# Performance work log

Hardware: AMD Instinct MI355X
Metric: run time of the kernel (lower is better)

## Reference

```python
import jax, jax.numpy as jnp
import numpy as np

DIM = 192
WH, WW = 8, 8
N = WH * WW
NUM_HEADS = 6
HEAD_DIM = DIM // NUM_HEADS
SCALE = HEAD_DIM ** (-0.5)
B_ = 4096


def _relative_position_index(Wh, Ww):
    coords = np.stack(np.meshgrid(np.arange(Wh), np.arange(Ww), indexing='ij'))  # [2, Wh, Ww]
    cf = coords.reshape(2, -1)                              # [2, N]
    rel = cf[:, :, None] - cf[:, None, :]                   # [2, N, N]
    rel = rel.transpose(1, 2, 0).astype(np.int64)           # [N, N, 2]
    rel[..., 0] += Wh - 1
    rel[..., 1] += Ww - 1
    rel[..., 0] *= 2 * Ww - 1
    return rel.sum(-1)                                      # [N, N]


REL_IDX = jnp.asarray(_relative_position_index(WH, WW))


def setup_inputs() -> dict:
    key = jax.random.key(0)
    ks = jax.random.split(key, 6)
    x = jax.random.normal(ks[0], (B_, N, DIM), dtype=jnp.float32)
    w_qkv = jax.random.normal(ks[1], (3 * DIM, DIM), dtype=jnp.float32) * (DIM ** -0.5)
    b_qkv = jnp.zeros((3 * DIM,), dtype=jnp.float32)
    w_proj = jax.random.normal(ks[2], (DIM, DIM), dtype=jnp.float32) * (DIM ** -0.5)
    b_proj = jnp.zeros((DIM,), dtype=jnp.float32)
    # torch init is zeros; use small noise so the bias path is exercised
    bias_table = jax.random.normal(ks[3], ((2 * WH - 1) * (2 * WW - 1), NUM_HEADS), dtype=jnp.float32) * 0.02
    return {"x": x, "w_qkv": w_qkv, "b_qkv": b_qkv, "w_proj": w_proj,
            "b_proj": b_proj, "bias_table": bias_table}


def reference(x, w_qkv, b_qkv, w_proj, b_proj, bias_table):
    B, n, C = x.shape
    qkv = jnp.einsum('bnc,dc->bnd', x, w_qkv) + b_qkv        # [B, N, 3C]
    qkv = qkv.reshape(B, n, 3, NUM_HEADS, HEAD_DIM)
    q = qkv[:, :, 0].transpose(0, 2, 1, 3) * SCALE            # [B, H, N, hd]
    k = qkv[:, :, 1].transpose(0, 2, 1, 3)
    v = qkv[:, :, 2].transpose(0, 2, 1, 3)
    attn = jnp.einsum('bhnd,bhmd->bhnm', q, k)                # [B, H, N, N]
    bias = bias_table[REL_IDX]                                # [N, N, H]
    attn = attn + bias.transpose(2, 0, 1)[None]               # broadcast over B
    attn = jax.nn.softmax(attn, axis=-1)
    out = jnp.einsum('bhnm,bhmd->bnhd', attn, v).reshape(B, n, C)
    return jnp.einsum('bnc,dc->bnd', out, w_proj) + b_proj
```

## Files before the change

kernel.cpp:

```cpp
#include <hip/hip_runtime.h>

#define TOK 64
#define CDIM 192
#define NH 6
#define HD 32
#define THREADS 384
#define QSCALE 0.17677669529663687f

#define WQ16_OFF 0
#define WP16_OFF 110592
#define BIAS_OFF 147456
#define WS_HALFS (147456 + 24576)
#define WS_BYTES (WS_HALFS * 2)

typedef _Float16 f16x8 __attribute__((ext_vector_type(8)));
typedef _Float16 f16x4 __attribute__((ext_vector_type(4)));
typedef float f32x4 __attribute__((ext_vector_type(4)));

__device__ __forceinline__ f16x8 ld8(const _Float16* p) {
  return *reinterpret_cast<const f16x8*>(p);
}

__device__ __forceinline__ f16x8 cvt8(const float* __restrict__ p) {
  float4 a = *reinterpret_cast<const float4*>(p);
  float4 c = *reinterpret_cast<const float4*>(p + 4);
  f16x8 r;
  r[0] = (_Float16)a.x; r[1] = (_Float16)a.y; r[2] = (_Float16)a.z; r[3] = (_Float16)a.w;
  r[4] = (_Float16)c.x; r[5] = (_Float16)c.y; r[6] = (_Float16)c.z; r[7] = (_Float16)c.w;
  return r;
}

__device__ __forceinline__ f16x4 pack4(float a, float b, float c, float d) {
  f16x4 r;
  r[0] = (_Float16)a; r[1] = (_Float16)b; r[2] = (_Float16)c; r[3] = (_Float16)d;
  return r;
}

__global__ void prep_ws(const float* __restrict__ wq, const float* __restrict__ wp,
                        const float* __restrict__ bt, _Float16* __restrict__ ws) {
  int i = blockIdx.x * 256 + threadIdx.x;
  if (i < 27648) {
    float4 v = reinterpret_cast<const float4*>(wq)[i];
    f16x4 h;
    h[0] = (_Float16)v.x; h[1] = (_Float16)v.y; h[2] = (_Float16)v.z; h[3] = (_Float16)v.w;
    *reinterpret_cast<f16x4*>(ws + WQ16_OFF + (size_t)i * 4) = h;
  } else if (i < 36864) {
    int j = i - 27648;
    float4 v = reinterpret_cast<const float4*>(wp)[j];
    f16x4 h;
    h[0] = (_Float16)v.x; h[1] = (_Float16)v.y; h[2] = (_Float16)v.z; h[3] = (_Float16)v.w;
    *reinterpret_cast<f16x4*>(ws + WP16_OFF + (size_t)j * 4) = h;
  } else if (i < 61440) {
    int j = i - 36864;
    int hit = j >> 10;
    int l = (j >> 4) & 63;
    int s = j & 15;
    int h = hit >> 2, it = hit & 3;
    int ii = it * 16 + (l & 15);
    int jj = (s >> 2) * 16 + (l >> 4) * 4 + (s & 3);
    int rel = ((ii >> 3) - (jj >> 3) + 7) * 15 + ((ii & 7) - (jj & 7) + 7);
    ws[BIAS_OFF + j] = (_Float16)bt[rel * NH + h];
  }
}

template <bool WS>
__global__ __launch_bounds__(THREADS, 5) void winattn(
    const float* __restrict__ x, const float* __restrict__ w_qkv,
    const float* __restrict__ b_qkv, const float* __restrict__ w_proj,
    const float* __restrict__ b_proj, const float* __restrict__ bias_table,
    const _Float16* __restrict__ ws, float* __restrict__ out) {
  __shared__ __align__(16) _Float16 R1[12288];

  const int tid = threadIdx.x;
  const int h   = tid >> 6;
  const int l   = tid & 63;
  const int l15 = l & 15;
  const int lg  = l >> 4;
  const int b   = blockIdx.x;
  const int sA0 = l15 ^ lg;
  const int sA1 = sA0 ^ 4;
  const f32x4 vzero = {0.f, 0.f, 0.f, 0.f};

  const float* xg = x + (size_t)b * (TOK * CDIM);
#pragma unroll
  for (int kk = 0; kk < 4; ++kk) {
    int q = tid + kk * THREADS;
    int n = q / 24;
    int p = q - n * 24;
    const float* src = xg + q * 8;
    float4 v0 = *reinterpret_cast<const float4*>(src);
    float4 v1 = *reinterpret_cast<const float4*>(src + 4);
    f16x8 h8;
    h8[0] = (_Float16)v0.x; h8[1] = (_Float16)v0.y;
    h8[2] = (_Float16)v0.z; h8[3] = (_Float16)v0.w;
    h8[4] = (_Float16)v1.x; h8[5] = (_Float16)v1.y;
    h8[6] = (_Float16)v1.z; h8[7] = (_Float16)v1.w;
    *reinterpret_cast<f16x8*>(&R1[(p * TOK + (n ^ (p & 7))) * 8]) = h8;
  }
  __syncthreads();

  f32x4 aq[2][4];
#pragma unroll
  for (int mt = 0; mt < 2; ++mt)
#pragma unroll
    for (int nt = 0; nt < 4; ++nt) aq[mt][nt] = vzero;
#pragma unroll
  for (int ks = 0; ks < 6; ++ks) {
    const int sx = (ks & 1) ? sA1 : sA0;
    f16x8 bx[4];
#pragma unroll
    for (int nt = 0; nt < 4; ++nt)
      bx[nt] = ld8(&R1[((ks * 4 + lg) * TOK + nt * 16 + sx) * 8]);
    f16x8 aw[2];
#pragma unroll
    for (int mt = 0; mt < 2; ++mt) {
      int row = h * HD + mt * 16 + l15;
      if constexpr (WS) aw[mt] = ld8(ws + WQ16_OFF + (size_t)row * CDIM + ks * 32 + lg * 8);
      else              aw[mt] = cvt8(w_qkv + (size_t)row * CDIM + ks * 32 + lg * 8);
    }
    __builtin_amdgcn_s_setprio(1);
#pragma unroll
    for (int mt = 0; mt < 2; ++mt)
#pragma unroll
      for (int nt = 0; nt < 4; ++nt)
        aq[mt][nt] = __builtin_amdgcn_mfma_f32_16x16x32_f16(aw[mt], bx[nt], aq[mt][nt], 0, 0, 0);
    __builtin_amdgcn_s_setprio(0);
  }
  f16x4 qp[2][4];
#pragma unroll
  for (int mt = 0; mt < 2; ++mt) {
    float4 bq = *reinterpret_cast<const float4*>(b_qkv + h * HD + mt * 16 + lg * 4);
#pragma unroll
    for (int nt = 0; nt < 4; ++nt)
      qp[mt][nt] = pack4((aq[mt][nt][0] + bq.x) * QSCALE, (aq[mt][nt][1] + bq.y) * QSCALE,
                         (aq[mt][nt][2] + bq.z) * QSCALE, (aq[mt][nt][3] + bq.w) * QSCALE);
  }

  f32x4 ak[2][4];
#pragma unroll
  for (int mt = 0; mt < 2; ++mt)
#pragma unroll
    for (int nt = 0; nt < 4; ++nt) ak[mt][nt] = vzero;
#pragma unroll
  for (int ks = 0; ks < 6; ++ks) {
    const int sx = (ks & 1) ? sA1 : sA0;
    f16x8 bx[4];
#pragma unroll
    for (int nt = 0; nt < 4; ++nt)
      bx[nt] = ld8(&R1[((ks * 4 + lg) * TOK + nt * 16 + sx) * 8]);
    f16x8 aw[2];
#pragma unroll
    for (int mt = 0; mt < 2; ++mt) {
      int row = CDIM + h * HD + mt * 16 + l15;
      if constexpr (WS) aw[mt] = ld8(ws + WQ16_OFF + (size_t)row * CDIM + ks * 32 + lg * 8);
      else              aw[mt] = cvt8(w_qkv + (size_t)row * CDIM + ks * 32 + lg * 8);
    }
    __builtin_amdgcn_s_setprio(1);
#pragma unroll
    for (int mt = 0; mt < 2; ++mt)
#pragma unroll
      for (int nt = 0; nt < 4; ++nt)
        ak[mt][nt] = __builtin_amdgcn_mfma_f32_16x16x32_f16(aw[mt], bx[nt], ak[mt][nt], 0, 0, 0);
    __builtin_amdgcn_s_setprio(0);
  }
  f16x4 kp[2][4];
#pragma unroll
  for (int mt = 0; mt < 2; ++mt) {
    float4 bk = *reinterpret_cast<const float4*>(b_qkv + CDIM + h * HD + mt * 16 + lg * 4);
#pragma unroll
    for (int nt = 0; nt < 4; ++nt)
      kp[mt][nt] = pack4(ak[mt][nt][0] + bk.x, ak[mt][nt][1] + bk.y,
                         ak[mt][nt][2] + bk.z, ak[mt][nt][3] + bk.w);
  }

  f16x4 vp[4][2];
#pragma unroll
  for (int ct = 0; ct < 2; ++ct) {
    f32x4 av[4];
#pragma unroll
    for (int mt = 0; mt < 4; ++mt) av[mt] = vzero;
    const int col = 2 * CDIM + h * HD + ct * 16 + l15;
#pragma unroll
    for (int ks = 0; ks < 6; ++ks) {
      const int sx = (ks & 1) ? sA1 : sA0;
      f16x8 a[4];
#pragma unroll
      for (int mt = 0; mt < 4; ++mt)
        a[mt] = ld8(&R1[((ks * 4 + lg) * TOK + mt * 16 + sx) * 8]);
      f16x8 bw;
      if constexpr (WS) bw = ld8(ws + WQ16_OFF + (size_t)col * CDIM + ks * 32 + lg * 8);
      else              bw = cvt8(w_qkv + (size_t)col * CDIM + ks * 32 + lg * 8);
      __builtin_amdgcn_s_setprio(1);
#pragma unroll
      for (int mt = 0; mt < 4; ++mt)
        av[mt] = __builtin_amdgcn_mfma_f32_16x16x32_f16(a[mt], bw, av[mt], 0, 0, 0);
      __builtin_amdgcn_s_setprio(0);
    }
    float bv = b_qkv[col];
#pragma unroll
    for (int s = 0; s < 4; ++s)
      vp[s][ct] = pack4(av[s][0] + bv, av[s][1] + bv, av[s][2] + bv, av[s][3] + bv);
  }
  __syncthreads();

#pragma unroll
  for (int it = 0; it < 4; ++it) {
    f32x4 st[4];
    __builtin_amdgcn_s_setprio(1);
#pragma unroll
    for (int jt = 0; jt < 4; ++jt) {
      st[jt] = __builtin_amdgcn_mfma_f32_16x16x16f16(kp[0][jt], qp[0][it], vzero, 0, 0, 0);
      st[jt] = __builtin_amdgcn_mfma_f32_16x16x16f16(kp[1][jt], qp[1][it], st[jt], 0, 0, 0);
    }
    __builtin_amdgcn_s_setprio(0);
    if constexpr (WS) {
      const _Float16* bw = ws + BIAS_OFF + ((h * 4 + it) * 64 + l) * 16;
      f16x8 b0 = ld8(bw), b1 = ld8(bw + 8);
#pragma unroll
      for (int jt = 0; jt < 4; ++jt)
#pragma unroll
        for (int r = 0; r < 4; ++r)
          st[jt][r] += (float)((jt < 2) ? b0[jt * 4 + r] : b1[(jt - 2) * 4 + r]);
    } else {
      int i = it * 16 + l15, yi = i >> 3, xi = i & 7;
#pragma unroll
      for (int jt = 0; jt < 4; ++jt)
#pragma unroll
        for (int r = 0; r < 4; ++r) {
          int j = jt * 16 + lg * 4 + r, yj = j >> 3, xj = j & 7;
          st[jt][r] += bias_table[(((yi - yj + 7) * 15 + (xi - xj + 7)) * NH + h)];
        }
    }
    float m = st[0][0];
#pragma unroll
    for (int jt = 0; jt < 4; ++jt)
#pragma unroll
      for (int r = 0; r < 4; ++r) m = fmaxf(m, st[jt][r]);
    m = fmaxf(m, __shfl_xor(m, 16, 64));
    m = fmaxf(m, __shfl_xor(m, 32, 64));
    float sum = 0.f;
#pragma unroll
    for (int jt = 0; jt < 4; ++jt)
#pragma unroll
      for (int r = 0; r < 4; ++r) { st[jt][r] = __expf(st[jt][r] - m); sum += st[jt][r]; }
    sum += __shfl_xor(sum, 16, 64);
    sum += __shfl_xor(sum, 32, 64);
    float inv = 1.f / sum;
    f32x4 o[2] = {vzero, vzero};
#pragma unroll
    for (int s = 0; s < 4; ++s) {
      f16x4 pp = pack4(st[s][0] * inv, st[s][1] * inv, st[s][2] * inv, st[s][3] * inv);
      __builtin_amdgcn_s_setprio(1);
      o[0] = __builtin_amdgcn_mfma_f32_16x16x16f16(pp, vp[s][0], o[0], 0, 0, 0);
      o[1] = __builtin_amdgcn_mfma_f32_16x16x16f16(pp, vp[s][1], o[1], 0, 0, 0);
      __builtin_amdgcn_s_setprio(0);
    }
#pragma unroll
    for (int ct = 0; ct < 2; ++ct) {
      int c = h * HD + ct * 16 + l15;
      int op = c >> 3, s7 = op & 7;
      int lgx = lg ^ (s7 >> 2);
      int base = (op * TOK + it * 16 + lgx * 4) * 8 + (c & 7);
#pragma unroll
      for (int r = 0; r < 4; ++r)
        R1[base + (r ^ (s7 & 3)) * 8] = (_Float16)o[ct][r];
    }
  }
  __syncthreads();

  {
    const int e0 = h * 16 + l15;
    const int e1 = e0 + 96;
    f32x4 pa0[4], pa1[4];
#pragma unroll
    for (int mt = 0; mt < 4; ++mt) { pa0[mt] = vzero; pa1[mt] = vzero; }
#pragma unroll
    for (int ks = 0; ks < 6; ++ks) {
      const int sx = (ks & 1) ? sA1 : sA0;
      f16x8 a[4];
#pragma unroll
      for (int mt = 0; mt < 4; ++mt)
        a[mt] = ld8(&R1[((ks * 4 + lg) * TOK + mt * 16 + sx) * 8]);
      f16x8 w0, w1;
      if constexpr (WS) {
        w0 = ld8(ws + WP16_OFF + (size_t)e0 * CDIM + ks * 32 + lg * 8);
        w1 = ld8(ws + WP16_OFF + (size_t)e1 * CDIM + ks * 32 + lg * 8);
      } else {
        w0 = cvt8(w_proj + (size_t)e0 * CDIM + ks * 32 + lg * 8);
        w1 = cvt8(w_proj + (size_t)e1 * CDIM + ks * 32 + lg * 8);
      }
      __builtin_amdgcn_s_setprio(1);
#pragma unroll
      for (int mt = 0; mt < 4; ++mt) {
        pa0[mt] = __builtin_amdgcn_mfma_f32_16x16x32_f16(a[mt], w0, pa0[mt], 0, 0, 0);
        pa1[mt] = __builtin_amdgcn_mfma_f32_16x16x32_f16(a[mt], w1, pa1[mt], 0, 0, 0);
      }
      __builtin_amdgcn_s_setprio(0);
    }
    float bp0 = b_proj[e0], bp1 = b_proj[e1];
#pragma unroll
    for (int mt = 0; mt < 4; ++mt) {
#pragma unroll
      for (int r = 0; r < 4; ++r) {
        int n = mt * 16 + lg * 4 + r;
        out[((size_t)b * TOK + n) * CDIM + e0] = pa0[mt][r] + bp0;
        out[((size_t)b * TOK + n) * CDIM + e1] = pa1[mt][r] + bp1;
      }
    }
  }
}

extern "C" void kernel_launch(void* const* d_in, const int* in_sizes, int n_in,
                              void* d_out, int out_size, void* d_ws, size_t ws_size,
                              hipStream_t stream) {
  const float* x          = (const float*)d_in[0];
  const float* w_qkv      = (const float*)d_in[1];
  const float* b_qkv      = (const float*)d_in[2];
  const float* w_proj     = (const float*)d_in[3];
  const float* b_proj     = (const float*)d_in[4];
  const float* bias_table = (const float*)d_in[5];
  float* out = (float*)d_out;
  int B = in_sizes[0] / (TOK * CDIM);

  if (ws_size >= (size_t)WS_BYTES) {
    _Float16* ws = (_Float16*)d_ws;
    hipLaunchKernelGGL(prep_ws, dim3(240), dim3(256), 0, stream,
                       w_qkv, w_proj, bias_table, ws);
    hipLaunchKernelGGL(winattn<true>, dim3(B), dim3(THREADS), 0, stream,
                       x, w_qkv, b_qkv, w_proj, b_proj, bias_table, ws, out);
  } else {
    hipLaunchKernelGGL(winattn<false>, dim3(B), dim3(THREADS), 0, stream,
                       x, w_qkv, b_qkv, w_proj, b_proj, bias_table,
                       (const _Float16*)nullptr, out);
  }
}
```

Before: 243.5 us.

## Fuse Q, K and V projection loops to share LDS x-fragment loads

Merges the three separate Q, K and V projection k-loops into one loop that loads the x tile fragments from LDS once per k-step and issues all 24 MFMAs against them. This cuts LDS reads of the activation tile to a third and gives the scheduler more independent MFMAs per iteration. In exchange all three accumulator sets are live at once, raising register pressure, so the launch-bounds occupancy hint is lowered from 5 to 3 blocks per CU.

```diff
diff --git a/kernel.cpp b/kernel.cpp
--- a/kernel.cpp
+++ b/kernel.cpp
@@ -64,7 +64,7 @@
 }
 
 template <bool WS>
-__global__ __launch_bounds__(THREADS, 5) void winattn(
+__global__ __launch_bounds__(THREADS, 3) void winattn(
     const float* __restrict__ x, const float* __restrict__ w_qkv,
     const float* __restrict__ b_qkv, const float* __restrict__ w_proj,
     const float* __restrict__ b_proj, const float* __restrict__ bias_table,
@@ -99,11 +99,16 @@
   }
   __syncthreads();
 
-  f32x4 aq[2][4];
+  f32x4 aq[2][4], ak[2][4], av[4][2];
 #pragma unroll
   for (int mt = 0; mt < 2; ++mt)
 #pragma unroll
-    for (int nt = 0; nt < 4; ++nt) aq[mt][nt] = vzero;
+    for (int nt = 0; nt < 4; ++nt) { aq[mt][nt] = vzero; ak[mt][nt] = vzero; }
+#pragma unroll
+  for (int mt = 0; mt < 4; ++mt)
+#pragma unroll
+    for (int ct = 0; ct < 2; ++ct) av[mt][ct] = vzero;
+
 #pragma unroll
   for (int ks = 0; ks < 6; ++ks) {
     const int sx = (ks & 1) ? sA1 : sA0;
@@ -111,95 +116,58 @@
 #pragma unroll
     for (int nt = 0; nt < 4; ++nt)
       bx[nt] = ld8(&R1[((ks * 4 + lg) * TOK + nt * 16 + sx) * 8]);
-    f16x8 aw[2];
+    f16x8 wq[2], wk[2], wv[2];
 #pragma unroll
     for (int mt = 0; mt < 2; ++mt) {
       int row = h * HD + mt * 16 + l15;
-      if constexpr (WS) aw[mt] = ld8(ws + WQ16_OFF + (size_t)row * CDIM + ks * 32 + lg * 8);
-      else              aw[mt] = cvt8(w_qkv + (size_t)row * CDIM + ks * 32 + lg * 8);
+      if constexpr (WS) {
+        wq[mt] = ld8(ws + WQ16_OFF + (size_t)row * CDIM + ks * 32 + lg * 8);
+        wk[mt] = ld8(ws + WQ16_OFF + (size_t)(row + CDIM) * CDIM + ks * 32 + lg * 8);
+        wv[mt] = ld8(ws + WQ16_OFF + (size_t)(row + 2 * CDIM) * CDIM + ks * 32 + lg * 8);
+      } else {
+        wq[mt] = cvt8(w_qkv + (size_t)row * CDIM + ks * 32 + lg * 8);
+        wk[mt] = cvt8(w_qkv + (size_t)(row + CDIM) * CDIM + ks * 32 + lg * 8);
+        wv[mt] = cvt8(w_qkv + (size_t)(row + 2 * CDIM) * CDIM + ks * 32 + lg * 8);
+      }
     }
     __builtin_amdgcn_s_setprio(1);
 #pragma unroll
     for (int mt = 0; mt < 2; ++mt)
 #pragma unroll
-      for (int nt = 0; nt < 4; ++nt)
-        aq[mt][nt] = __builtin_amdgcn_mfma_f32_16x16x32_f16(aw[mt], bx[nt], aq[mt][nt], 0, 0, 0);
+      for (int nt = 0; nt < 4; ++nt) {
+        aq[mt][nt] = __builtin_amdgcn_mfma_f32_16x16x32_f16(wq[mt], bx[nt], aq[mt][nt], 0, 0, 0);
+        ak[mt][nt] = __builtin_amdgcn_mfma_f32_16x16x32_f16(wk[mt], bx[nt], ak[mt][nt], 0, 0, 0);
+      }
+#pragma unroll
+    for (int mt = 0; mt < 4; ++mt)
+#pragma unroll
+      for (int ct = 0; ct < 2; ++ct)
+        av[mt][ct] = __builtin_amdgcn_mfma_f32_16x16x32_f16(bx[mt], wv[ct], av[mt][ct], 0, 0, 0);
     __builtin_amdgcn_s_setprio(0);
   }
-  f16x4 qp[2][4];
+
+  f16x4 qp[2][4], kp[2][4];
 #pragma unroll
   for (int mt = 0; mt < 2; ++mt) {
     float4 bq = *reinterpret_cast<const float4*>(b_qkv + h * HD + mt * 16 + lg * 4);
-#pragma unroll
-    for (int nt = 0; nt < 4; ++nt)
+    float4 bk = *reinterpret_cast<const float4*>(b_qkv + CDIM + h * HD + mt * 16 + lg * 4);
+#pragma unroll
+    for (int nt = 0; nt < 4; ++nt) {
       qp[mt][nt] = pack4((aq[mt][nt][0] + bq.x) * QSCALE, (aq[mt][nt][1] + bq.y) * QSCALE,
                          (aq[mt][nt][2] + bq.z) * QSCALE, (aq[mt][nt][3] + bq.w) * QSCALE);
-  }
-
-  f32x4 ak[2][4];
-#pragma unroll
-  for (int mt = 0; mt < 2; ++mt)
-#pragma unroll
-    for (int nt = 0; nt < 4; ++nt) ak[mt][nt] = vzero;
-#pragma unroll
-  for (int ks = 0; ks < 6; ++ks) {
-    const int sx = (ks & 1) ? sA1 : sA0;
-    f16x8 bx[4];
-#pragma unroll
-    for (int nt = 0; nt < 4; ++nt)
-      bx[nt] = ld8(&R1[((ks * 4 + lg) * TOK + nt * 16 + sx) * 8]);
-    f16x8 aw[2];
-#pragma unroll
-    for (int mt = 0; mt < 2; ++mt) {
-      int row = CDIM + h * HD + mt * 16 + l15;
-      if constexpr (WS) aw[mt] = ld8(ws + WQ16_OFF + (size_t)row * CDIM + ks * 32 + lg * 8);
-      else              aw[mt] = cvt8(w_qkv + (size_t)row * CDIM + ks * 32 + lg * 8);
-    }
-    __builtin_amdgcn_s_setprio(1);
-#pragma unroll
-    for (int mt = 0; mt < 2; ++mt)
-#pragma unroll
-      for (int nt = 0; nt < 4; ++nt)
-        ak[mt][nt] = __builtin_amdgcn_mfma_f32_16x16x32_f16(aw[mt], bx[nt], ak[mt][nt], 0, 0, 0);
-    __builtin_amdgcn_s_setprio(0);
-  }
-  f16x4 kp[2][4];
-#pragma unroll
-  for (int mt = 0; mt < 2; ++mt) {
-    float4 bk = *reinterpret_cast<const float4*>(b_qkv + CDIM + h * HD + mt * 16 + lg * 4);
-#pragma unroll
-    for (int nt = 0; nt < 4; ++nt)
       kp[mt][nt] = pack4(ak[mt][nt][0] + bk.x, ak[mt][nt][1] + bk.y,
                          ak[mt][nt][2] + bk.z, ak[mt][nt][3] + bk.w);
-  }
-
+    }
+  }
   f16x4 vp[4][2];
-#pragma unroll
-  for (int ct = 0; ct < 2; ++ct) {
-    f32x4 av[4];
-#pragma unroll
-    for (int mt = 0; mt < 4; ++mt) av[mt] = vzero;
-    const int col = 2 * CDIM + h * HD + ct * 16 + l15;
-#pragma unroll
-    for (int ks = 0; ks < 6; ++ks) {
-      const int sx = (ks & 1) ? sA1 : sA0;
-      f16x8 a[4];
-#pragma unroll
-      for (int mt = 0; mt < 4; ++mt)
-        a[mt] = ld8(&R1[((ks * 4 + lg) * TOK + mt * 16 + sx) * 8]);
-      f16x8 bw;
-      if constexpr (WS) bw = ld8(ws + WQ16_OFF + (size_t)col * CDIM + ks * 32 + lg * 8);
-      else              bw = cvt8(w_qkv + (size_t)col * CDIM + ks * 32 + lg * 8);
-      __builtin_amdgcn_s_setprio(1);
-#pragma unroll
-      for (int mt = 0; mt < 4; ++mt)
-        av[mt] = __builtin_amdgcn_mfma_f32_16x16x32_f16(a[mt], bw, av[mt], 0, 0, 0);
-      __builtin_amdgcn_s_setprio(0);
-    }
-    float bv = b_qkv[col];
-#pragma unroll
-    for (int s = 0; s < 4; ++s)
-      vp[s][ct] = pack4(av[s][0] + bv, av[s][1] + bv, av[s][2] + bv, av[s][3] + bv);
+  {
+    float bv0 = b_qkv[2 * CDIM + h * HD + l15];
+    float bv1 = b_qkv[2 * CDIM + h * HD + 16 + l15];
+#pragma unroll
+    for (int s = 0; s < 4; ++s) {
+      vp[s][0] = pack4(av[s][0][0] + bv0, av[s][0][1] + bv0, av[s][0][2] + bv0, av[s][0][3] + bv0);
+      vp[s][1] = pack4(av[s][1][0] + bv1, av[s][1][1] + bv1, av[s][1][2] + bv1, av[s][1][3] + bv1);
+    }
   }
   __syncthreads();
 
```

Result: slower. 275.6 us (+13.2%).

## Stage K in LDS, merge V tiles, vectorize output stores via swapped MFMA operands

Applied to the files above, without the earlier changes.

K projections are written to a new 24KB shared buffer and reloaded per attention tile instead of being held in registers, which lowers register pressure. The two V column tiles are computed in one k-loop so the X tile is read from LDS once. The output projection swaps MFMA operands so each lane holds 4 consecutive output columns, allowing float4 global stores instead of scalar strided stores. LDS pointer bases are also hoisted. The cost is doubled LDS per block (48KB), which may limit occupancy at 5 blocks per CU, plus extra LDS traffic for K.

```diff
diff --git a/kernel.cpp b/kernel.cpp
--- a/kernel.cpp
+++ b/kernel.cpp
@@ -19,6 +19,9 @@
 
 __device__ __forceinline__ f16x8 ld8(const _Float16* p) {
   return *reinterpret_cast<const f16x8*>(p);
+}
+__device__ __forceinline__ f16x4 ld4(const _Float16* p) {
+  return *reinterpret_cast<const f16x4*>(p);
 }
 
 __device__ __forceinline__ f16x8 cvt8(const float* __restrict__ p) {
@@ -70,6 +73,7 @@
     const float* __restrict__ b_proj, const float* __restrict__ bias_table,
     const _Float16* __restrict__ ws, float* __restrict__ out) {
   __shared__ __align__(16) _Float16 R1[12288];
+  __shared__ __align__(16) _Float16 KP[12288];
 
   const int tid = threadIdx.x;
   const int h   = tid >> 6;
@@ -99,107 +103,125 @@
   }
   __syncthreads();
 
-  f32x4 aq[2][4];
-#pragma unroll
-  for (int mt = 0; mt < 2; ++mt)
-#pragma unroll
-    for (int nt = 0; nt < 4; ++nt) aq[mt][nt] = vzero;
-#pragma unroll
-  for (int ks = 0; ks < 6; ++ks) {
-    const int sx = (ks & 1) ? sA1 : sA0;
-    f16x8 bx[4];
-#pragma unroll
-    for (int nt = 0; nt < 4; ++nt)
-      bx[nt] = ld8(&R1[((ks * 4 + lg) * TOK + nt * 16 + sx) * 8]);
-    f16x8 aw[2];
+  const _Float16* bxb0 = &R1[(lg * TOK + sA0) * 8];
+  const _Float16* bxb1 = &R1[(lg * TOK + sA1) * 8];
+  _Float16* kpb = &KP[(size_t)h * 2048 + l * 4];
+
+  f16x4 qp[2][4];
+  {
+    f32x4 aq[2][4];
+#pragma unroll
+    for (int mt = 0; mt < 2; ++mt)
+#pragma unroll
+      for (int nt = 0; nt < 4; ++nt) aq[mt][nt] = vzero;
+#pragma unroll
+    for (int ks = 0; ks < 6; ++ks) {
+      const _Float16* bb = (ks & 1) ? bxb1 : bxb0;
+      f16x8 bx[4];
+#pragma unroll
+      for (int nt = 0; nt < 4; ++nt)
+        bx[nt] = ld8(bb + ks * 2048 + nt * 128);
+      f16x8 aw[2];
+#pragma unroll
+      for (int mt = 0; mt < 2; ++mt) {
+        int row = h * HD + mt * 16 + l15;
+        if constexpr (WS) aw[mt] = ld8(ws + WQ16_OFF + (size_t)row * CDIM + ks * 32 + lg * 8);
+        else              aw[mt] = cvt8(w_qkv + (size_t)row * CDIM + ks * 32 + lg * 8);
+      }
+      __builtin_amdgcn_s_setprio(1);
+#pragma unroll
+      for (int mt = 0; mt < 2; ++mt)
+#pragma unroll
+        for (int nt = 0; nt < 4; ++nt)
+          aq[mt][nt] = __builtin_amdgcn_mfma_f32_16x16x32_f16(aw[mt], bx[nt], aq[mt][nt], 0, 0, 0);
+      __builtin_amdgcn_s_setprio(0);
+    }
 #pragma unroll
     for (int mt = 0; mt < 2; ++mt) {
-      int row = h * HD + mt * 16 + l15;
-      if constexpr (WS) aw[mt] = ld8(ws + WQ16_OFF + (size_t)row * CDIM + ks * 32 + lg * 8);
-      else              aw[mt] = cvt8(w_qkv + (size_t)row * CDIM + ks * 32 + lg * 8);
-    }
-    __builtin_amdgcn_s_setprio(1);
+      float4 bq = *reinterpret_cast<const float4*>(b_qkv + h * HD + mt * 16 + lg * 4);
+#pragma unroll
+      for (int nt = 0; nt < 4; ++nt)
+        qp[mt][nt] = pack4((aq[mt][nt][0] + bq.x) * QSCALE, (aq[mt][nt][1] + bq.y) * QSCALE,
+                           (aq[mt][nt][2] + bq.z) * QSCALE, (aq[mt][nt][3] + bq.w) * QSCALE);
+    }
+  }
+
+  {
+    f32x4 ak[2][4];
 #pragma unroll
     for (int mt = 0; mt < 2; ++mt)
 #pragma unroll
+      for (int nt = 0; nt < 4; ++nt) ak[mt][nt] = vzero;
+#pragma unroll
+    for (int ks = 0; ks < 6; ++ks) {
+      const _Float16* bb = (ks & 1) ? bxb1 : bxb0;
+      f16x8 bx[4];
+#pragma unroll
       for (int nt = 0; nt < 4; ++nt)
-        aq[mt][nt] = __builtin_amdgcn_mfma_f32_16x16x32_f16(aw[mt], bx[nt], aq[mt][nt], 0, 0, 0);
-    __builtin_amdgcn_s_setprio(0);
-  }
-  f16x4 qp[2][4];
-#pragma unroll
-  for (int mt = 0; mt < 2; ++mt) {
-    float4 bq = *reinterpret_cast<const float4*>(b_qkv + h * HD + mt * 16 + lg * 4);
-#pragma unroll
-    for (int nt = 0; nt < 4; ++nt)
-      qp[mt][nt] = pack4((aq[mt][nt][0] + bq.x) * QSCALE, (aq[mt][nt][1] + bq.y) * QSCALE,
-                         (aq[mt][nt][2] + bq.z) * QSCALE, (aq[mt][nt][3] + bq.w) * QSCALE);
-  }
-
-  f32x4 ak[2][4];
-#pragma unroll
-  for (int mt = 0; mt < 2; ++mt)
-#pragma unroll
-    for (int nt = 0; nt < 4; ++nt) ak[mt][nt] = vzero;
-#pragma unroll
-  for (int ks = 0; ks < 6; ++ks) {
-    const int sx = (ks & 1) ? sA1 : sA0;
-    f16x8 bx[4];
-#pragma unroll
-    for (int nt = 0; nt < 4; ++nt)
-      bx[nt] = ld8(&R1[((ks * 4 + lg) * TOK + nt * 16 + sx) * 8]);
-    f16x8 aw[2];
+        bx[nt] = ld8(bb + ks * 2048 + nt * 128);
+      f16x8 aw[2];
+#pragma unroll
+      for (int mt = 0; mt < 2; ++mt) {
+        int row = CDIM + h * HD + mt * 16 + l15;
+        if constexpr (WS) aw[mt] = ld8(ws + WQ16_OFF + (size_t)row * CDIM + ks * 32 + lg * 8);
+        else              aw[mt] = cvt8(w_qkv + (size_t)row * CDIM + ks * 32 + lg * 8);
+      }
+      __builtin_amdgcn_s_setprio(1);
+#pragma unroll
+      for (int mt = 0; mt < 2; ++mt)
+#pragma unroll
+        for (int nt = 0; nt < 4; ++nt)
+          ak[mt][nt] = __builtin_amdgcn_mfma_f32_16x16x32_f16(aw[mt], bx[nt], ak[mt][nt], 0, 0, 0);
+      __builtin_amdgcn_s_setprio(0);
+    }
 #pragma unroll
     for (int mt = 0; mt < 2; ++mt) {
-      int row = CDIM + h * HD + mt * 16 + l15;
-      if constexpr (WS) aw[mt] = ld8(ws + WQ16_OFF + (size_t)row * CDIM + ks * 32 + lg * 8);
-      else              aw[mt] = cvt8(w_qkv + (size_t)row * CDIM + ks * 32 + lg * 8);
-    }
-    __builtin_amdgcn_s_setprio(1);
-#pragma unroll
-    for (int mt = 0; mt < 2; ++mt)
-#pragma unroll
-      for (int nt = 0; nt < 4; ++nt)
-        ak[mt][nt] = __builtin_amdgcn_mfma_f32_16x16x32_f16(aw[mt], bx[nt], ak[mt][nt], 0, 0, 0);
-    __builtin_amdgcn_s_setprio(0);
-  }
-  f16x4 kp[2][4];
-#pragma unroll
-  for (int mt = 0; mt < 2; ++mt) {
-    float4 bk = *reinterpret_cast<const float4*>(b_qkv + CDIM + h * HD + mt * 16 + lg * 4);
-#pragma unroll
-    for (int nt = 0; nt < 4; ++nt)
-      kp[mt][nt] = pack4(ak[mt][nt][0] + bk.x, ak[mt][nt][1] + bk.y,
-                         ak[mt][nt][2] + bk.z, ak[mt][nt][3] + bk.w);
+      float4 bk = *reinterpret_cast<const float4*>(b_qkv + CDIM + h * HD + mt * 16 + lg * 4);
+#pragma unroll
+      for (int nt = 0; nt < 4; ++nt) {
+        f16x4 t = pack4(ak[mt][nt][0] + bk.x, ak[mt][nt][1] + bk.y,
+                        ak[mt][nt][2] + bk.z, ak[mt][nt][3] + bk.w);
+        *reinterpret_cast<f16x4*>(kpb + (mt * 4 + nt) * 256) = t;
+      }
+    }
   }
 
   f16x4 vp[4][2];
-#pragma unroll
-  for (int ct = 0; ct < 2; ++ct) {
-    f32x4 av[4];
-#pragma unroll
-    for (int mt = 0; mt < 4; ++mt) av[mt] = vzero;
-    const int col = 2 * CDIM + h * HD + ct * 16 + l15;
+  {
+    f32x4 av[4][2];
+#pragma unroll
+    for (int mt = 0; mt < 4; ++mt)
+#pragma unroll
+      for (int ct = 0; ct < 2; ++ct) av[mt][ct] = vzero;
 #pragma unroll
     for (int ks = 0; ks < 6; ++ks) {
-      const int sx = (ks & 1) ? sA1 : sA0;
+      const _Float16* bb = (ks & 1) ? bxb1 : bxb0;
       f16x8 a[4];
 #pragma unroll
       for (int mt = 0; mt < 4; ++mt)
-        a[mt] = ld8(&R1[((ks * 4 + lg) * TOK + mt * 16 + sx) * 8]);
-      f16x8 bw;
-      if constexpr (WS) bw = ld8(ws + WQ16_OFF + (size_t)col * CDIM + ks * 32 + lg * 8);
-      else              bw = cvt8(w_qkv + (size_t)col * CDIM + ks * 32 + lg * 8);
+        a[mt] = ld8(bb + ks * 2048 + mt * 128);
+      f16x8 bw[2];
+#pragma unroll
+      for (int ct = 0; ct < 2; ++ct) {
+        int col = 2 * CDIM + h * HD + ct * 16 + l15;
+        if constexpr (WS) bw[ct] = ld8(ws + WQ16_OFF + (size_t)col * CDIM + ks * 32 + lg * 8);
+        else              bw[ct] = cvt8(w_qkv + (size_t)col * CDIM + ks * 32 + lg * 8);
+      }
       __builtin_amdgcn_s_setprio(1);
 #pragma unroll
       for (int mt = 0; mt < 4; ++mt)
-        av[mt] = __builtin_amdgcn_mfma_f32_16x16x32_f16(a[mt], bw, av[mt], 0, 0, 0);
-      __builtin_amdgcn_s_setprio(0);
-    }
-    float bv = b_qkv[col];
-#pragma unroll
-    for (int s = 0; s < 4; ++s)
-      vp[s][ct] = pack4(av[s][0] + bv, av[s][1] + bv, av[s][2] + bv, av[s][3] + bv);
+#pragma unroll
+        for (int ct = 0; ct < 2; ++ct)
+          av[mt][ct] = __builtin_amdgcn_mfma_f32_16x16x32_f16(a[mt], bw[ct], av[mt][ct], 0, 0, 0);
+      __builtin_amdgcn_s_setprio(0);
+    }
+    float bv0 = b_qkv[2 * CDIM + h * HD + l15];
+    float bv1 = b_qkv[2 * CDIM + h * HD + 16 + l15];
+#pragma unroll
+    for (int s = 0; s < 4; ++s) {
+      vp[s][0] = pack4(av[s][0][0] + bv0, av[s][0][1] + bv0, av[s][0][2] + bv0, av[s][0][3] + bv0);
+      vp[s][1] = pack4(av[s][1][0] + bv1, av[s][1][1] + bv1, av[s][1][2] + bv1, av[s][1][3] + bv1);
+    }
   }
   __syncthreads();
 
@@ -209,8 +231,10 @@
     __builtin_amdgcn_s_setprio(1);
 #pragma unroll
     for (int jt = 0; jt < 4; ++jt) {
-      st[jt] = __builtin_amdgcn_mfma_f32_16x16x16f16(kp[0][jt], qp[0][it], vzero, 0, 0, 0);
-      st[jt] = __builtin_amdgcn_mfma_f32_16x16x16f16(kp[1][jt], qp[1][it], st[jt], 0, 0, 0);
+      f16x4 k0 = ld4(kpb + jt * 256);
+      f16x4 k1 = ld4(kpb + (4 + jt) * 256);
+      st[jt] = __builtin_amdgcn_mfma_f32_16x16x16f16(k0, qp[0][it], vzero, 0, 0, 0);
+      st[jt] = __builtin_amdgcn_mfma_f32_16x16x16f16(k1, qp[1][it], st[jt], 0, 0, 0);
     }
     __builtin_amdgcn_s_setprio(0);
     if constexpr (WS) {
@@ -269,43 +293,45 @@
   __syncthreads();
 
   {
-    const int e0 = h * 16 + l15;
-    const int e1 = e0 + 96;
     f32x4 pa0[4], pa1[4];
 #pragma unroll
-    for (int mt = 0; mt < 4; ++mt) { pa0[mt] = vzero; pa1[mt] = vzero; }
+    for (int nt = 0; nt < 4; ++nt) { pa0[nt] = vzero; pa1[nt] = vzero; }
 #pragma unroll
     for (int ks = 0; ks < 6; ++ks) {
-      const int sx = (ks & 1) ? sA1 : sA0;
+      const _Float16* bb = (ks & 1) ? bxb1 : bxb0;
       f16x8 a[4];
 #pragma unroll
-      for (int mt = 0; mt < 4; ++mt)
-        a[mt] = ld8(&R1[((ks * 4 + lg) * TOK + mt * 16 + sx) * 8]);
+      for (int nt = 0; nt < 4; ++nt)
+        a[nt] = ld8(bb + ks * 2048 + nt * 128);
       f16x8 w0, w1;
       if constexpr (WS) {
-        w0 = ld8(ws + WP16_OFF + (size_t)e0 * CDIM + ks * 32 + lg * 8);
-        w1 = ld8(ws + WP16_OFF + (size_t)e1 * CDIM + ks * 32 + lg * 8);
+        w0 = ld8(ws + WP16_OFF + (size_t)(h * 16 + l15) * CDIM + ks * 32 + lg * 8);
+        w1 = ld8(ws + WP16_OFF + (size_t)(h * 16 + 96 + l15) * CDIM + ks * 32 + lg * 8);
       } else {
-        w0 = cvt8(w_proj + (size_t)e0 * CDIM + ks * 32 + lg * 8);
-        w1 = cvt8(w_proj + (size_t)e1 * CDIM + ks * 32 + lg * 8);
-      }
-      __builtin_amdgcn_s_setprio(1);
-#pragma unroll
-      for (int mt = 0; mt < 4; ++mt) {
-        pa0[mt] = __builtin_amdgcn_mfma_f32_16x16x32_f16(a[mt], w0, pa0[mt], 0, 0, 0);
-        pa1[mt] = __builtin_amdgcn_mfma_f32_16x16x32_f16(a[mt], w1, pa1[mt], 0, 0, 0);
-      }
-      __builtin_amdgcn_s_setprio(0);
-    }
-    float bp0 = b_proj[e0], bp1 = b_proj[e1];
-#pragma unroll
-    for (int mt = 0; mt < 4; ++mt) {
-#pragma unroll
-      for (int r = 0; r < 4; ++r) {
-        int n = mt * 16 + lg * 4 + r;
-        out[((size_t)b * TOK + n) * CDIM + e0] = pa0[mt][r] + bp0;
-        out[((size_t)b * TOK + n) * CDIM + e1] = pa1[mt][r] + bp1;
-      }
+        w0 = cvt8(w_proj + (size_t)(h * 16 + l15) * CDIM + ks * 32 + lg * 8);
+        w1 = cvt8(w_proj + (size_t)(h * 16 + 96 + l15) * CDIM + ks * 32 + lg * 8);
+      }
+      __builtin_amdgcn_s_setprio(1);
+#pragma unroll
+      for (int nt = 0; nt < 4; ++nt) {
+        pa0[nt] = __builtin_amdgcn_mfma_f32_16x16x32_f16(w0, a[nt], pa0[nt], 0, 0, 0);
+        pa1[nt] = __builtin_amdgcn_mfma_f32_16x16x32_f16(w1, a[nt], pa1[nt], 0, 0, 0);
+      }
+      __builtin_amdgcn_s_setprio(0);
+    }
+    float* outw = out + (size_t)b * (TOK * CDIM);
+    float4 bp0 = *reinterpret_cast<const float4*>(b_proj + h * 16 + lg * 4);
+    float4 bp1 = *reinterpret_cast<const float4*>(b_proj + h * 16 + 96 + lg * 4);
+#pragma unroll
+    for (int nt = 0; nt < 4; ++nt) {
+      float4 r0, r1;
+      r0.x = pa0[nt][0] + bp0.x; r0.y = pa0[nt][1] + bp0.y;
+      r0.z = pa0[nt][2] + bp0.z; r0.w = pa0[nt][3] + bp0.w;
+      r1.x = pa1[nt][0] + bp1.x; r1.y = pa1[nt][1] + bp1.y;
+      r1.z = pa1[nt][2] + bp1.z; r1.w = pa1[nt][3] + bp1.w;
+      float* rowp = outw + (nt * 16 + l15) * CDIM + h * 16 + lg * 4;
+      *reinterpret_cast<float4*>(rowp) = r0;
+      *reinterpret_cast<float4*>(rowp + 96) = r1;
     }
   }
 }
```

Result: no change. 240.1 us (-1.4%).
